# Kernel tuning notes

Measured on AMD Instinct MI355X. Metric: run time of the kernel, lower is better.

The kernel has to match this reference:

```python
import jax, jax.numpy as jnp
import numpy as np

VOCAB = 10000
EMB = 512
D_IMG = 2048
RNN = 1024
SEQ_LEN = 16
START_TOKEN = VOCAB + 1  # 10001
V_OUT = VOCAB + 3        # 10003


def setup_inputs() -> dict:
    key = jax.random.key(0)
    ks = jax.random.split(key, 24)
    g = lambda k, shape, fan_in: jax.random.normal(k, shape, jnp.float32) / np.sqrt(fan_in)
    inp = {
        "img_features": jax.random.normal(ks[0], (64, 196, D_IMG), jnp.float32),
        "captions": jax.random.randint(ks[1], (64, SEQ_LEN), 0, VOCAB),
        # embedding table
        "emb": g(ks[2], (V_OUT, EMB), EMB),
        # LSTMCell (PyTorch gate order i,f,g,o), stored as [in, 4H]
        "Wih": g(ks[3], (EMB + D_IMG, 4 * RNN), EMB + D_IMG),
        "Whh": g(ks[4], (RNN, 4 * RNN), RNN),
        "bih": jnp.zeros((4 * RNN,), jnp.float32),
        "bhh": jnp.zeros((4 * RNN,), jnp.float32),
        # init_h / init_c
        "Wh0": g(ks[5], (D_IMG, RNN), D_IMG), "bh0": jnp.zeros((RNN,), jnp.float32),
        "Wc0": g(ks[6], (D_IMG, RNN), D_IMG), "bc0": jnp.zeros((RNN,), jnp.float32),
        # f_beta gate
        "Wfb": g(ks[7], (RNN, D_IMG), RNN), "bfb": jnp.zeros((D_IMG,), jnp.float32),
        # deep_output
        "Wout": g(ks[8], (RNN, V_OUT), RNN), "bout": jnp.zeros((V_OUT,), jnp.float32),
        # attention: U (rnn->rnn), W (img->rnn), v (rnn->1)
        "WU": g(ks[9], (RNN, RNN), RNN), "bU": jnp.zeros((RNN,), jnp.float32),
        "WW": g(ks[10], (D_IMG, RNN), D_IMG), "bW": jnp.zeros((RNN,), jnp.float32),
        "Wv": g(ks[11], (RNN, 1), RNN), "bv": jnp.zeros((1,), jnp.float32),
    }
    return inp


def reference(img_features, captions, emb, Wih, Whh, bih, bhh, Wh0, bh0, Wc0, bc0,
              Wfb, bfb, Wout, bout, WU, bU, WW, bW, Wv, bv):
    B = img_features.shape[0]
    # get_target: prepend START token -> [B, T+1]
    start = jnp.full((B, 1), START_TOKEN, dtype=captions.dtype)
    target = jnp.concatenate([start, captions], axis=1)
    embedding = emb[target]                      # [B, T+1, EMB]
    emb_seq = jnp.transpose(embedding, (1, 0, 2))  # [T+1, B, EMB]

    # init LSTM state from mean image features
    avg = img_features.mean(axis=1)              # [B, D_IMG]
    h0 = jnp.tanh(avg @ Wh0 + bh0)
    c0 = jnp.tanh(avg @ Wc0 + bc0)

    # image-side attention projection is timestep-independent
    W_s = img_features @ WW + bW                 # [B, L, RNN]
    b_gates = bih + bhh

    def step(carry, emb_t):
        h, c = carry
        # additive attention
        U_h = h @ WU + bU                        # [B, RNN]
        att = jnp.tanh(W_s + U_h[:, None, :])    # [B, L, RNN]
        e = (att @ Wv).squeeze(-1) + bv          # [B, L]
        alpha = jax.nn.softmax(e, axis=1)
        context = jnp.einsum('bld,bl->bd', img_features, alpha)  # [B, D_IMG]
        gate = jax.nn.sigmoid(h @ Wfb + bfb)
        x = jnp.concatenate([emb_t, gate * context], axis=1)     # [B, EMB+D_IMG]
        # LSTMCell, PyTorch gate order i,f,g,o
        gates = x @ Wih + h @ Whh + b_gates      # [B, 4*RNN]
        i, f, gg, o = jnp.split(gates, 4, axis=1)
        c_new = jax.nn.sigmoid(f) * c + jax.nn.sigmoid(i) * jnp.tanh(gg)
        h_new = jax.nn.sigmoid(o) * jnp.tanh(c_new)
        out = h_new @ Wout + bout                # [B, V_OUT] (dropout=identity, eval mode)
        return (h_new, c_new), (out, alpha)

    (_, _), (preds_t, alphas_t) = jax.lax.scan(step, (h0, c0), emb_seq)
    preds = jnp.transpose(preds_t, (1, 0, 2))    # [B, T+1, V_OUT]
    alphas = jnp.transpose(alphas_t, (1, 0, 2))  # [B, T+1, L]
    return preds, alphas
```

## Files before the change

### kernel.cpp

```cpp
#include <hip/hip_runtime.h>
#include <cstdint>

#define NB    64
#define LIMG  196
#define DIMG  2048
#define RNND  1024
#define EMBD  512
#define TSTEPS 17
#define VOUTD 10003

typedef short bf16x8 __attribute__((ext_vector_type(8)));
typedef float f32x4  __attribute__((ext_vector_type(4)));

__device__ __forceinline__ float fast_sig(float x) {
    return 1.f / (1.f + __expf(-x));
}
__device__ __forceinline__ float fast_tanh(float x) {
    float ax = fabsf(x);
    float e  = __expf(2.f * ax);
    float r  = 1.f - 2.f / (e + 1.f);
    return copysignf(r, x);
}
__device__ __forceinline__ void split_bf(float x, short& hi, short& lo) {
    unsigned u  = __float_as_uint(x);
    unsigned hb = u & 0xffff0000u;
    hi = (short)(u >> 16);
    float r = x - __uint_as_float(hb);
    lo = (short)(__float_as_uint(r) >> 16);
}

__global__ __launch_bounds__(256) void tsplit(
    const float* __restrict__ S1, int ld1,
    const float* __restrict__ S2, int ld2,
    short* __restrict__ outh, short* __restrict__ outl,
    int N, int K, int ksplit, int nsplit)
{
    __shared__ float T[64][65];
    const int k0 = blockIdx.x * 64, n0 = blockIdx.y * 64;
    const int tid = threadIdx.x;
    const int rr = tid >> 2;
    const int cc = (tid & 3) * 16;
    const int kk = k0 + rr;
    const int nn = n0 + cc;
    const float* rp; int col;
    if (nsplit > 0) {
        if (nn >= nsplit) { rp = S2 + (size_t)kk * ld2; col = nn - nsplit; }
        else              { rp = S1 + (size_t)kk * ld1; col = nn; }
    } else {
        if (kk < ksplit)  { rp = S1 + (size_t)kk * ld1; col = nn; }
        else              { rp = S2 + (size_t)(kk - ksplit) * ld2; col = nn; }
    }
#pragma unroll
    for (int j = 0; j < 16; j++)
        T[rr][cc + j] = (nn + j < N) ? rp[col + j] : 0.f;
    __syncthreads();
    const int wn = tid >> 2;
    const int wk = (tid & 3) * 16;
    const int gn = n0 + wn;
    if (gn >= N) return;
    bf16x8 h0, h1, l0, l1;
#pragma unroll
    for (int j = 0; j < 8; j++) {
        short hh, ll;
        split_bf(T[wk + j][wn], hh, ll);     h0[j] = hh; l0[j] = ll;
        split_bf(T[wk + 8 + j][wn], hh, ll); h1[j] = hh; l1[j] = ll;
    }
    const size_t o = (size_t)gn * K + k0 + wk;
    *(bf16x8*)&outh[o]     = h0;
    *(bf16x8*)&outh[o + 8] = h1;
    *(bf16x8*)&outl[o]     = l0;
    *(bf16x8*)&outl[o + 8] = l1;
}

__global__ __launch_bounds__(256) void gemm_mt(
    const float* __restrict__ Af,
    const short* __restrict__ Ah16, const short* __restrict__ Al16,
    const short* __restrict__ Bh16, const short* __restrict__ Bl16,
    const float* __restrict__ bias, float* __restrict__ C,
    int N, int K, int lda, int ldb, int ldc, int pmap)
{
    __shared__ short Ah[64 * 40], Al[64 * 40];
    __shared__ short Bh[128 * 40], Bl[128 * 40];

    const int tid = threadIdx.x;
    const int n0  = blockIdx.x * 128;
    const int m0  = blockIdx.y * 64;

    const int lane = tid & 63;
    const int w    = tid >> 6;
    const int wn   = w * 32;
    const int lm   = lane & 15;
    const int lk   = lane >> 4;

    const int a_r = tid >> 2;
    const int a_c = (tid & 3) * 8;
    const int b_r = tid >> 1;
    const int b_c = (tid & 1) * 16;

    f32x4 acc[4][2];
#pragma unroll
    for (int i = 0; i < 4; i++)
#pragma unroll
        for (int j = 0; j < 2; j++) acc[i][j] = (f32x4)0.f;

    bf16x8 rah, ral, rbh0, rbh1, rbl0, rbl1;
    auto load_tile = [&](int k0) {
        if (Af) {
            const float* ap = Af + (size_t)(m0 + a_r) * lda + (k0 + a_c);
            float4 q0 = *(const float4*)(ap);
            float4 q1 = *(const float4*)(ap + 4);
            float f[8] = {q0.x, q0.y, q0.z, q0.w, q1.x, q1.y, q1.z, q1.w};
#pragma unroll
            for (int j = 0; j < 8; j++) {
                short hh, ll;
                split_bf(f[j], hh, ll); rah[j] = hh; ral[j] = ll;
            }
        } else {
            rah = *(const bf16x8*)(Ah16 + (size_t)(m0 + a_r) * lda + (k0 + a_c));
            ral = *(const bf16x8*)(Al16 + (size_t)(m0 + a_r) * lda + (k0 + a_c));
        }
        const short* pb = Bh16 + (size_t)(n0 + b_r) * ldb + (k0 + b_c);
        rbh0 = *(const bf16x8*)pb; rbh1 = *(const bf16x8*)(pb + 8);
        const short* qb = Bl16 + (size_t)(n0 + b_r) * ldb + (k0 + b_c);
        rbl0 = *(const bf16x8*)qb; rbl1 = *(const bf16x8*)(qb + 8);
    };

    load_tile(0);
    for (int k0 = 0; k0 < K; k0 += 32) {
        __syncthreads();
        *(bf16x8*)&Ah[a_r * 40 + a_c] = rah;
        *(bf16x8*)&Al[a_r * 40 + a_c] = ral;
        *(bf16x8*)&Bh[b_r * 40 + b_c]     = rbh0;
        *(bf16x8*)&Bh[b_r * 40 + b_c + 8] = rbh1;
        *(bf16x8*)&Bl[b_r * 40 + b_c]     = rbl0;
        *(bf16x8*)&Bl[b_r * 40 + b_c + 8] = rbl1;
        __syncthreads();
        if (k0 + 32 < K) load_tile(k0 + 32);

        bf16x8 afh[4], afl[4], bfh[2], bfl[2];
#pragma unroll
        for (int fm = 0; fm < 4; fm++) {
            const int idx = (fm * 16 + lm) * 40 + lk * 8;
            afh[fm] = *(bf16x8*)&Ah[idx];
            afl[fm] = *(bf16x8*)&Al[idx];
        }
#pragma unroll
        for (int fn = 0; fn < 2; fn++) {
            const int idx = (wn + fn * 16 + lm) * 40 + lk * 8;
            bfh[fn] = *(bf16x8*)&Bh[idx];
            bfl[fn] = *(bf16x8*)&Bl[idx];
        }
#pragma unroll
        for (int fm = 0; fm < 4; fm++)
#pragma unroll
            for (int fn = 0; fn < 2; fn++) {
                acc[fm][fn] = __builtin_amdgcn_mfma_f32_16x16x32_bf16(afh[fm], bfh[fn], acc[fm][fn], 0, 0, 0);
                acc[fm][fn] = __builtin_amdgcn_mfma_f32_16x16x32_bf16(afh[fm], bfl[fn], acc[fm][fn], 0, 0, 0);
                acc[fm][fn] = __builtin_amdgcn_mfma_f32_16x16x32_bf16(afl[fm], bfh[fn], acc[fm][fn], 0, 0, 0);
            }
    }

#pragma unroll
    for (int fm = 0; fm < 4; fm++)
#pragma unroll
        for (int fn = 0; fn < 2; fn++) {
            const int col = n0 + wn + fn * 16 + lm;
            if (col >= N) continue;
            const float bb = bias ? bias[col] : 0.f;
#pragma unroll
            for (int r = 0; r < 4; r++) {
                const int row = m0 + fm * 16 + lk * 4 + r;
                const size_t orow = pmap ? (size_t)((row & 63) * TSTEPS + (row >> 6))
                                         : (size_t)row;
                C[orow * ldc + col] = acc[fm][fn][r] + bb;
            }
        }
}

__global__ __launch_bounds__(256) void gemm_sk(
    const float* __restrict__ A,
    const short* __restrict__ Bh16, const short* __restrict__ Bl16,
    float* __restrict__ P, int N, int K, int lda, int ldb, int Kc)
{
    __shared__ short Ah[64 * 40], Al[64 * 40];
    __shared__ short Bh[128 * 40], Bl[128 * 40];

    const int tid = threadIdx.x;
    const int n0  = blockIdx.x * 128;
    const int s   = blockIdx.z;
    const int kb  = s * Kc;

    const int lane = tid & 63;
    const int w    = tid >> 6;
    const int wn   = w * 32;
    const int lm   = lane & 15;
    const int lk   = lane >> 4;

    const int a_r = tid >> 2;
    const int a_c = (tid & 3) * 8;
    const int b_r = tid >> 1;
    const int b_c = (tid & 1) * 16;

    f32x4 acc[4][2];
#pragma unroll
    for (int i = 0; i < 4; i++)
#pragma unroll
        for (int j = 0; j < 2; j++) acc[i][j] = (f32x4)0.f;

    for (int k0 = kb; k0 < kb + Kc; k0 += 32) {
        const float* ap = A + (size_t)a_r * lda + (k0 + a_c);
        float4 q0 = *(const float4*)(ap);
        float4 q1 = *(const float4*)(ap + 4);
        float f[8] = {q0.x, q0.y, q0.z, q0.w, q1.x, q1.y, q1.z, q1.w};
        bf16x8 ah, al;
#pragma unroll
        for (int j = 0; j < 8; j++) {
            short hh, ll;
            split_bf(f[j], hh, ll); ah[j] = hh; al[j] = ll;
        }
        const short* pb = Bh16 + (size_t)(n0 + b_r) * ldb + (k0 + b_c);
        bf16x8 bh0 = *(const bf16x8*)pb, bh1 = *(const bf16x8*)(pb + 8);
        const short* qb = Bl16 + (size_t)(n0 + b_r) * ldb + (k0 + b_c);
        bf16x8 bl0 = *(const bf16x8*)qb, bl1 = *(const bf16x8*)(qb + 8);

        __syncthreads();
        *(bf16x8*)&Ah[a_r * 40 + a_c] = ah;
        *(bf16x8*)&Al[a_r * 40 + a_c] = al;
        *(bf16x8*)&Bh[b_r * 40 + b_c]     = bh0;
        *(bf16x8*)&Bh[b_r * 40 + b_c + 8] = bh1;
        *(bf16x8*)&Bl[b_r * 40 + b_c]     = bl0;
        *(bf16x8*)&Bl[b_r * 40 + b_c + 8] = bl1;
        __syncthreads();

        bf16x8 afh[4], afl[4], bfh[2], bfl[2];
#pragma unroll
        for (int fm = 0; fm < 4; fm++) {
            const int idx = (fm * 16 + lm) * 40 + lk * 8;
            afh[fm] = *(bf16x8*)&Ah[idx];
            afl[fm] = *(bf16x8*)&Al[idx];
        }
#pragma unroll
        for (int fn = 0; fn < 2; fn++) {
            const int idx = (wn + fn * 16 + lm) * 40 + lk * 8;
            bfh[fn] = *(bf16x8*)&Bh[idx];
            bfl[fn] = *(bf16x8*)&Bl[idx];
        }
#pragma unroll
        for (int fm = 0; fm < 4; fm++)
#pragma unroll
            for (int fn = 0; fn < 2; fn++) {
                acc[fm][fn] = __builtin_amdgcn_mfma_f32_16x16x32_bf16(afh[fm], bfh[fn], acc[fm][fn], 0, 0, 0);
                acc[fm][fn] = __builtin_amdgcn_mfma_f32_16x16x32_bf16(afh[fm], bfl[fn], acc[fm][fn], 0, 0, 0);
                acc[fm][fn] = __builtin_amdgcn_mfma_f32_16x16x32_bf16(afl[fm], bfh[fn], acc[fm][fn], 0, 0, 0);
            }
    }

    float* Ps = P + (size_t)s * 64 * N;
#pragma unroll
    for (int fm = 0; fm < 4; fm++)
#pragma unroll
        for (int fn = 0; fn < 2; fn++) {
            const int col = n0 + wn + fn * 16 + lm;
#pragma unroll
            for (int r = 0; r < 4; r++) {
                const int row = fm * 16 + lk * 4 + r;
                Ps[(size_t)row * N + col] = acc[fm][fn][r];
            }
        }
}

__global__ __launch_bounds__(256) void gemm64(
    const float* __restrict__ A, const float* __restrict__ B,
    const float* __restrict__ bias, float* __restrict__ C,
    int N, int K, int Kc, int ldc, int act, int direct)
{
    __shared__ float As[16][64];
    __shared__ float Bs[16][68];

    const int tid = threadIdx.x;
    const int n0  = blockIdx.x * 64;
    const int m0  = blockIdx.y * 64;
    const int s   = blockIdx.z;
    const int kb  = s * Kc;
    const int ke  = min(K, kb + Kc);

    const int tm = (tid >> 4) << 2;
    const int tn = (tid & 15) << 2;

    float acc[4][4];
#pragma unroll
    for (int i = 0; i < 4; i++)
#pragma unroll
        for (int j = 0; j < 4; j++) acc[i][j] = 0.f;

    const int a_m = tid >> 2;
    const int a_k = (tid & 3) << 2;
    const int b_k = tid >> 4;
    const int b_n = (tid & 15) << 2;
    const bool n4 = ((N & 3) == 0);

    for (int k0 = kb; k0 < ke; k0 += 16) {
        float4 av = *(const float4*)(A + (size_t)(m0 + a_m) * K + (k0 + a_k));
        float4 bv;
        {
            const int nn = n0 + b_n;
            const float* brow = B + (size_t)(k0 + b_k) * N;
            if (n4) {
                bv = (nn < N) ? *(const float4*)(brow + nn) : make_float4(0.f,0.f,0.f,0.f);
            } else {
                bv.x = (nn + 0 < N) ? brow[nn + 0] : 0.f;
                bv.y = (nn + 1 < N) ? brow[nn + 1] : 0.f;
                bv.z = (nn + 2 < N) ? brow[nn + 2] : 0.f;
                bv.w = (nn + 3 < N) ? brow[nn + 3] : 0.f;
            }
        }
        __syncthreads();
        As[a_k + 0][a_m] = av.x;
        As[a_k + 1][a_m] = av.y;
        As[a_k + 2][a_m] = av.z;
        As[a_k + 3][a_m] = av.w;
        *(float4*)&Bs[b_k][b_n] = bv;
        __syncthreads();
#pragma unroll
        for (int k = 0; k < 16; k++) {
            float4 a4 = *(const float4*)&As[k][tm];
            float4 b4 = *(const float4*)&Bs[k][tn];
            acc[0][0] = fmaf(a4.x, b4.x, acc[0][0]);
            acc[0][1] = fmaf(a4.x, b4.y, acc[0][1]);
            acc[0][2] = fmaf(a4.x, b4.z, acc[0][2]);
            acc[0][3] = fmaf(a4.x, b4.w, acc[0][3]);
            acc[1][0] = fmaf(a4.y, b4.x, acc[1][0]);
            acc[1][1] = fmaf(a4.y, b4.y, acc[1][1]);
            acc[1][2] = fmaf(a4.y, b4.z, acc[1][2]);
            acc[1][3] = fmaf(a4.y, b4.w, acc[1][3]);
            acc[2][0] = fmaf(a4.z, b4.x, acc[2][0]);
            acc[2][1] = fmaf(a4.z, b4.y, acc[2][1]);
            acc[2][2] = fmaf(a4.z, b4.z, acc[2][2]);
            acc[2][3] = fmaf(a4.z, b4.w, acc[2][3]);
            acc[3][0] = fmaf(a4.w, b4.x, acc[3][0]);
            acc[3][1] = fmaf(a4.w, b4.y, acc[3][1]);
            acc[3][2] = fmaf(a4.w, b4.z, acc[3][2]);
            acc[3][3] = fmaf(a4.w, b4.w, acc[3][3]);
        }
    }

    if (direct) {
#pragma unroll
        for (int i = 0; i < 4; i++) {
            const int m = m0 + tm + i;
            const size_t row = (size_t)m * ldc;
#pragma unroll
            for (int j = 0; j < 4; j++) {
                const int n = n0 + tn + j;
                if (n < N) {
                    float v = acc[i][j] + (bias ? bias[n] : 0.f);
                    if (act == 1) v = fast_tanh(v);
                    else if (act == 2) v = fast_sig(v);
                    C[row + n] = v;
                }
            }
        }
    } else {
        float* Pp = C + (size_t)s * 64 * N;
#pragma unroll
        for (int i = 0; i < 4; i++) {
#pragma unroll
            for (int j = 0; j < 4; j++) {
                const int n = n0 + tn + j;
                if (n < N) Pp[(size_t)(tm + i) * N + n] = acc[i][j];
            }
        }
    }
}

__global__ __launch_bounds__(256) void gemm_mfma3(
    const float* __restrict__ A, const float* __restrict__ B,
    const float* __restrict__ bias, float* __restrict__ C,
    int M, int N, int K, int lda, int ldb, int ldc, int pmap)
{
    __shared__ short Ah[128 * 40], Al[128 * 40];
    __shared__ short Bh[128 * 40], Bl[128 * 40];

    const int tid = threadIdx.x;
    const int n0  = blockIdx.x * 128;
    const int m0  = blockIdx.y * 128;

    const int lane = tid & 63;
    const int w    = tid >> 6;
    const int wm   = (w >> 1) * 64;
    const int wn   = (w & 1) * 64;
    const int lm   = lane & 15;
    const int lk   = lane >> 4;

    const int ar = tid >> 1;
    const int ac = (tid & 1) * 16;
    const int kb = (tid & 15) * 2;
    const int c8 = (tid >> 4) * 8;

    const bool bvec = ((ldb & 3) == 0) && (n0 + 128 <= N);

    f32x4 acc[4][4];
#pragma unroll
    for (int i = 0; i < 4; i++)
#pragma unroll
        for (int j = 0; j < 4; j++) acc[i][j] = (f32x4)0.f;

    for (int k0 = 0; k0 < K; k0 += 32) {
        float f[16];
        if (m0 + ar < M) {
            const float* ap = A + (size_t)(m0 + ar) * lda + (k0 + ac);
            float4 q0 = *(const float4*)(ap);
            float4 q1 = *(const float4*)(ap + 4);
            float4 q2 = *(const float4*)(ap + 8);
            float4 q3 = *(const float4*)(ap + 12);
            f[0]=q0.x; f[1]=q0.y; f[2]=q0.z; f[3]=q0.w;
            f[4]=q1.x; f[5]=q1.y; f[6]=q1.z; f[7]=q1.w;
            f[8]=q2.x; f[9]=q2.y; f[10]=q2.z; f[11]=q2.w;
            f[12]=q3.x; f[13]=q3.y; f[14]=q3.z; f[15]=q3.w;
        } else {
#pragma unroll
            for (int j = 0; j < 16; j++) f[j] = 0.f;
        }
        bf16x8 h0, h1, l0, l1;
#pragma unroll
        for (int j = 0; j < 8; j++) {
            short hh, ll;
            split_bf(f[j], hh, ll);     h0[j] = hh; l0[j] = ll;
            split_bf(f[8 + j], hh, ll); h1[j] = hh; l1[j] = ll;
        }
        float g0[8], g1[8];
        if (bvec) {
            const float* bp0 = B + (size_t)(k0 + kb) * ldb + (n0 + c8);
            const float* bp1 = bp0 + ldb;
            float4 q0 = *(const float4*)(bp0);
            float4 q1 = *(const float4*)(bp0 + 4);
            float4 q2 = *(const float4*)(bp1);
            float4 q3 = *(const float4*)(bp1 + 4);
            g0[0]=q0.x; g0[1]=q0.y; g0[2]=q0.z; g0[3]=q0.w;
            g0[4]=q1.x; g0[5]=q1.y; g0[6]=q1.z; g0[7]=q1.w;
            g1[0]=q2.x; g1[1]=q2.y; g1[2]=q2.z; g1[3]=q2.w;
            g1[4]=q3.x; g1[5]=q3.y; g1[6]=q3.z; g1[7]=q3.w;
        } else {
            const float* bp0 = B + (size_t)(k0 + kb) * ldb;
            const float* bp1 = bp0 + ldb;
#pragma unroll
            for (int j = 0; j < 8; j++) {
                const int nn = n0 + c8 + j;
                g0[j] = (nn < N) ? bp0[nn] : 0.f;
                g1[j] = (nn < N) ? bp1[nn] : 0.f;
            }
        }
        __syncthreads();
        *(bf16x8*)&Ah[ar * 40 + ac]     = h0;
        *(bf16x8*)&Ah[ar * 40 + ac + 8] = h1;
        *(bf16x8*)&Al[ar * 40 + ac]     = l0;
        *(bf16x8*)&Al[ar * 40 + ac + 8] = l1;
#pragma unroll
        for (int j = 0; j < 8; j++) {
            short ha, la, hb, lb;
            split_bf(g0[j], ha, la);
            split_bf(g1[j], hb, lb);
            const int ci = (c8 + j) * 40 + kb;
            *(int*)&Bh[ci] = (int)((unsigned short)ha | ((unsigned)(unsigned short)hb << 16));
            *(int*)&Bl[ci] = (int)((unsigned short)la | ((unsigned)(unsigned short)lb << 16));
        }
        __syncthreads();

        bf16x8 afh[4], afl[4], bfh[4], bfl[4];
#pragma unroll
        for (int fm = 0; fm < 4; fm++) {
            const int idx = (wm + fm * 16 + lm) * 40 + lk * 8;
            afh[fm] = *(bf16x8*)&Ah[idx];
            afl[fm] = *(bf16x8*)&Al[idx];
        }
#pragma unroll
        for (int fn = 0; fn < 4; fn++) {
            const int idx = (wn + fn * 16 + lm) * 40 + lk * 8;
            bfh[fn] = *(bf16x8*)&Bh[idx];
            bfl[fn] = *(bf16x8*)&Bl[idx];
        }
#pragma unroll
        for (int fm = 0; fm < 4; fm++)
#pragma unroll
            for (int fn = 0; fn < 4; fn++) {
                acc[fm][fn] = __builtin_amdgcn_mfma_f32_16x16x32_bf16(afh[fm], bfh[fn], acc[fm][fn], 0, 0, 0);
                acc[fm][fn] = __builtin_amdgcn_mfma_f32_16x16x32_bf16(afh[fm], bfl[fn], acc[fm][fn], 0, 0, 0);
                acc[fm][fn] = __builtin_amdgcn_mfma_f32_16x16x32_bf16(afl[fm], bfh[fn], acc[fm][fn], 0, 0, 0);
            }
    }

#pragma unroll
    for (int fm = 0; fm < 4; fm++) {
#pragma unroll
        for (int fn = 0; fn < 4; fn++) {
            const int col = n0 + wn + fn * 16 + lm;
            if (col >= N) continue;
            const float bb = bias ? bias[col] : 0.f;
#pragma unroll
            for (int r = 0; r < 4; r++) {
                const int row = m0 + wm + fm * 16 + lk * 4 + r;
                if (row >= M) continue;
                const size_t orow = pmap ? (size_t)((row & 63) * TSTEPS + (row >> 6))
                                         : (size_t)row;
                C[orow * ldc + col] = acc[fm][fn][r] + bb;
            }
        }
    }
}

__global__ __launch_bounds__(256) void reduce_partials(
    const float* __restrict__ P, int S, int N,
    const float* __restrict__ bias, float* __restrict__ C, int ldc, int act)
{
    const int idx = blockIdx.x * 256 + threadIdx.x;
    const int total = 64 * N;
    if (idx >= total) return;
    const int m = idx / N;
    const int n = idx - m * N;
    float v = bias ? bias[n] : 0.f;
    for (int s = 0; s < S; s++) v += P[(size_t)s * total + idx];
    if (act == 1) v = fast_tanh(v);
    else if (act == 2) v = fast_sig(v);
    else if (act == 3 && n >= RNND) v = fast_sig(v);
    C[(size_t)m * ldc + n] = v;
}

__global__ __launch_bounds__(256) void reduce_lstm(
    const float* __restrict__ P, int S, const float* __restrict__ bsum,
    float* __restrict__ hn, float* __restrict__ c,
    short* __restrict__ hbh, short* __restrict__ hbl)
{
    const int idx = blockIdx.x * 256 + threadIdx.x;
    const int b = idx >> 10, r = idx & 1023;
    const float* pb = P + (size_t)b * 4096;
    float gi = bsum[r], gf = bsum[1024 + r], gg = bsum[2048 + r], go = bsum[3072 + r];
    for (int s = 0; s < S; s++) {
        const float* q = pb + (size_t)s * 64 * 4096;
        gi += q[r]; gf += q[1024 + r]; gg += q[2048 + r]; go += q[3072 + r];
    }
    const float ig = fast_sig(gi);
    const float fg = fast_sig(gf);
    const float g2 = fast_tanh(gg);
    const float og = fast_sig(go);
    const float cn = fg * c[idx] + ig * g2;
    const float hv = og * fast_tanh(cn);
    c[idx]  = cn;
    hn[idx] = hv;
    if (hbh) {
        short hi, lo;
        split_bf(hv, hi, lo);
        hbh[idx] = hi;
        hbl[idx] = lo;
    }
}

__global__ __launch_bounds__(256) void mean_img(
    const float* __restrict__ img, float* __restrict__ avg)
{
    const int b = blockIdx.x;
    const int d = blockIdx.y * 256 + threadIdx.x;
    const float* p = img + (size_t)b * LIMG * DIMG + d;
    float s = 0.f;
    for (int l = 0; l < LIMG; l++) s += p[(size_t)l * DIMG];
    avg[(size_t)b * DIMG + d] = s * (1.f / 196.f);
}

__global__ __launch_bounds__(256) void concat_w(
    const float* __restrict__ WU, const float* __restrict__ Wfb,
    float* __restrict__ Wug)
{
    const int idx = blockIdx.x * 256 + threadIdx.x;
    if (idx >= 1024 * 3072) return;
    const int k = idx / 3072;
    const int j = idx - k * 3072;
    Wug[idx] = (j < 1024) ? WU[(size_t)k * 1024 + j] : Wfb[(size_t)k * 2048 + (j - 1024)];
}

__global__ __launch_bounds__(256) void concat_b(
    const float* __restrict__ bU, const float* __restrict__ bfb,
    const float* __restrict__ bih, const float* __restrict__ bhh,
    float* __restrict__ bug, float* __restrict__ bsum)
{
    const int j = blockIdx.x * 256 + threadIdx.x;
    if (j < 3072) bug[j] = (j < 1024) ? bU[j] : bfb[j - 1024];
    if (j < 4096) bsum[j] = bih[j] + bhh[j];
}

__global__ __launch_bounds__(256) void attn_e(
    const float* __restrict__ Ws, const float* __restrict__ ug,
    const float* __restrict__ Wv, const float* __restrict__ bv,
    float* __restrict__ e)
{
    const int wv   = (blockIdx.x << 2) + (threadIdx.x >> 6);
    const int lane = threadIdx.x & 63;
    const int b    = wv / LIMG;
    const float* wrow = Ws + (size_t)wv * RNND;
    const float* urow = ug + (size_t)b * 3072;
    float acc = 0.f;
#pragma unroll
    for (int k = lane * 4; k < RNND; k += 256) {
        float4 wq = *(const float4*)(wrow + k);
        float4 uq = *(const float4*)(urow + k);
        float4 vq = *(const float4*)(Wv + k);
        acc += fast_tanh(wq.x + uq.x) * vq.x + fast_tanh(wq.y + uq.y) * vq.y
             + fast_tanh(wq.z + uq.z) * vq.z + fast_tanh(wq.w + uq.w) * vq.w;
    }
#pragma unroll
    for (int off = 32; off > 0; off >>= 1) acc += __shfl_down(acc, off);
    if (lane == 0) e[wv] = acc + bv[0];
}

__global__ __launch_bounds__(256) void ctx_fuse(
    const float* __restrict__ e, const float* __restrict__ img,
    const float* __restrict__ ug, const float* __restrict__ embt,
    const int* __restrict__ captions, const float* __restrict__ h,
    float* __restrict__ x, float* __restrict__ alphas_out, int t)
{
    __shared__ float al[256];
    __shared__ float red[256];
    const int b = blockIdx.x, y = blockIdx.y, tid = threadIdx.x;

    const float v = (tid < LIMG) ? e[b * LIMG + tid] : -3.0e38f;
    red[tid] = v; __syncthreads();
    for (int s = 128; s > 0; s >>= 1) {
        if (tid < s) red[tid] = fmaxf(red[tid], red[tid + s]);
        __syncthreads();
    }
    const float mx = red[0]; __syncthreads();
    const float ex = (tid < LIMG) ? __expf(v - mx) : 0.f;
    red[tid] = ex; __syncthreads();
    for (int s = 128; s > 0; s >>= 1) {
        if (tid < s) red[tid] += red[tid + s];
        __syncthreads();
    }
    const float inv = 1.f / red[0];
    al[tid] = ex * inv;
    __syncthreads();

    if (y == 0) {
        if (tid < LIMG)
            alphas_out[(size_t)b * (TSTEPS * LIMG) + t * LIMG + tid] = al[tid];
        const int tok = (t == 0) ? 10001 : captions[b * 16 + (t - 1)];
        for (int j = tid; j < EMBD; j += 256)
            x[(size_t)b * 3584 + j] = embt[(size_t)tok * EMBD + j];
        for (int j = tid; j < RNND; j += 256)
            x[(size_t)b * 3584 + 2560 + j] = h[(size_t)b * RNND + j];
    } else {
        const int d0 = (y - 1) * 512 + tid * 2;
        const float* ib = img + (size_t)b * LIMG * DIMG + d0;
        float a0 = 0.f, a1 = 0.f;
#pragma unroll 4
        for (int l = 0; l < LIMG; l++) {
            float2 q = *(const float2*)(ib + (size_t)l * DIMG);
            a0 = fmaf(al[l], q.x, a0);
            a1 = fmaf(al[l], q.y, a1);
        }
        const float g0 = ug[(size_t)b * 3072 + 1024 + d0];
        const float g1 = ug[(size_t)b * 3072 + 1024 + d0 + 1];
        x[(size_t)b * 3584 + EMBD + d0]     = g0 * a0;
        x[(size_t)b * 3584 + EMBD + d0 + 1] = g1 * a1;
    }
}

__global__ __launch_bounds__(256) void softmax_alpha(
    const float* __restrict__ e, float* __restrict__ alpha,
    float* __restrict__ alphas_out, int t)
{
    __shared__ float red[256];
    const int b = blockIdx.x, tid = threadIdx.x;
    const float v = (tid < LIMG) ? e[b * LIMG + tid] : -3.0e38f;
    red[tid] = v; __syncthreads();
    for (int s = 128; s > 0; s >>= 1) {
        if (tid < s) red[tid] = fmaxf(red[tid], red[tid + s]);
        __syncthreads();
    }
    const float mx = red[0]; __syncthreads();
    const float ex = (tid < LIMG) ? __expf(v - mx) : 0.f;
    red[tid] = ex; __syncthreads();
    for (int s = 128; s > 0; s >>= 1) {
        if (tid < s) red[tid] += red[tid + s];
        __syncthreads();
    }
    const float inv = 1.f / red[0];
    if (tid < LIMG) {
        const float a = ex * inv;
        alpha[b * LIMG + tid] = a;
        alphas_out[(size_t)b * (TSTEPS * LIMG) + t * LIMG + tid] = a;
    }
}

__global__ __launch_bounds__(128) void assemble_x(
    const float* __restrict__ img, const float* __restrict__ alpha,
    const float* __restrict__ ug, const float* __restrict__ emb,
    const int* __restrict__ captions, const float* __restrict__ h,
    float* __restrict__ x, int t, int stride)
{
    const int b = blockIdx.x, y = blockIdx.y, tid = threadIdx.x;
    if (y < 4) {
        const int tok = (t == 0) ? 10001 : captions[b * 16 + (t - 1)];
        const int j = y * 128 + tid;
        x[(size_t)b * stride + j] = emb[(size_t)tok * EMBD + j];
    } else if (y < 20) {
        __shared__ float al[LIMG];
        for (int i = tid; i < LIMG; i += 128) al[i] = alpha[b * LIMG + i];
        __syncthreads();
        const int d = (y - 4) * 128 + tid;
        const float* ib = img + (size_t)b * LIMG * DIMG + d;
        float accv = 0.f;
#pragma unroll 4
        for (int l = 0; l < LIMG; l++) accv = fmaf(al[l], ib[(size_t)l * DIMG], accv);
        const float g = ug[(size_t)b * 3072 + 1024 + d];
        x[(size_t)b * stride + EMBD + d] = g * accv;
    } else {
        const int j = (y - 20) * 128 + tid;
        x[(size_t)b * stride + 2560 + j] = h[(size_t)b * RNND + j];
    }
}

extern "C" void kernel_launch(void* const* d_in, const int* in_sizes, int n_in,
                              void* d_out, int out_size, void* d_ws, size_t ws_size,
                              hipStream_t stream)
{
    const float* img      = (const float*)d_in[0];
    const int*   captions = (const int*)d_in[1];
    const float* emb      = (const float*)d_in[2];
    const float* Wih      = (const float*)d_in[3];
    const float* Whh      = (const float*)d_in[4];
    const float* bih      = (const float*)d_in[5];
    const float* bhh      = (const float*)d_in[6];
    const float* Wh0      = (const float*)d_in[7];
    const float* bh0      = (const float*)d_in[8];
    const float* Wc0      = (const float*)d_in[9];
    const float* bc0      = (const float*)d_in[10];
    const float* Wfb      = (const float*)d_in[11];
    const float* bfb      = (const float*)d_in[12];
    const float* Wout     = (const float*)d_in[13];
    const float* bout     = (const float*)d_in[14];
    const float* WU       = (const float*)d_in[15];
    const float* bU       = (const float*)d_in[16];
    const float* WW       = (const float*)d_in[17];
    const float* bW       = (const float*)d_in[18];
    const float* Wv       = (const float*)d_in[19];
    const float* bv       = (const float*)d_in[20];

    float* preds      = (float*)d_out;
    float* alphas_out = preds + (size_t)NB * TSTEPS * VOUTD;

    const size_t NEED = 190000000;

    if (ws_size >= NEED) {
        float* w = (float*)d_ws;
        float* Ws    = w; w += (size_t)12544 * 1024;
        float* ug    = w; w += (size_t)64 * 3072;
        float* P     = w; w += (size_t)8 * 64 * 4096;
        float* e     = w; w += (size_t)64 * LIMG;
        float* alpha = w; w += (size_t)64 * LIMG;
        float* xh    = w; w += (size_t)64 * 3584;
        float* h     = w; w += (size_t)64 * RNND;
        float* c     = w; w += (size_t)64 * RNND;
        float* avg   = w; w += (size_t)64 * DIMG;
        float* bsum  = w; w += 4096;
        float* bug   = w; w += 3072;
        short* u = (short*)w;
        short* Hbh     = u; u += (size_t)1280 * 1024;
        short* Hbl     = u; u += (size_t)1280 * 1024;
        short* WWTh    = u; u += (size_t)1024 * 2048;
        short* WWTl    = u; u += (size_t)1024 * 2048;
        short* WugTh   = u; u += (size_t)3072 * 1024;
        short* WugTl   = u; u += (size_t)3072 * 1024;
        short* WfullTh = u; u += (size_t)4096 * 3584;
        short* WfullTl = u; u += (size_t)4096 * 3584;
        short* WoutTh  = u; u += (size_t)10112 * 1024;
        short* WoutTl  = u; u += (size_t)10112 * 1024;

        mean_img<<<dim3(NB, 8), 256, 0, stream>>>(img, avg);
        gemm64<<<dim3(16, 1, 8), 256, 0, stream>>>(avg, Wh0, nullptr, P, 1024, 2048, 256, 0, 0, 0);
        reduce_partials<<<256, 256, 0, stream>>>(P, 8, 1024, bh0, h, 1024, 1);
        gemm64<<<dim3(16, 1, 8), 256, 0, stream>>>(avg, Wc0, nullptr, P, 1024, 2048, 256, 0, 0, 0);
        reduce_partials<<<256, 256, 0, stream>>>(P, 8, 1024, bc0, c, 1024, 1);
        concat_b<<<16, 256, 0, stream>>>(bU, bfb, bih, bhh, bug, bsum);

        tsplit<<<dim3(32, 16), 256, 0, stream>>>(WW, 1024, WW, 1024, WWTh, WWTl, 1024, 2048, 2048, 0);
        tsplit<<<dim3(16, 48), 256, 0, stream>>>(WU, 1024, Wfb, 2048, WugTh, WugTl, 3072, 1024, 1024, 1024);
        tsplit<<<dim3(56, 64), 256, 0, stream>>>(Wih, 4096, Whh, 4096, WfullTh, WfullTl, 4096, 3584, 2560, 0);
        tsplit<<<dim3(16, 157), 256, 0, stream>>>(Wout, VOUTD, Wout, VOUTD, WoutTh, WoutTl, VOUTD, 1024, 1024, 0);

        gemm_mt<<<dim3(8, 196), 256, 0, stream>>>(img, nullptr, nullptr, WWTh, WWTl,
                                                  bW, Ws, 1024, 2048, 2048, 2048, 1024, 0);

        for (int t = 0; t < TSTEPS; t++) {
            gemm_sk<<<dim3(24, 1, 8), 256, 0, stream>>>(h, WugTh, WugTl, P, 3072, 1024, 1024, 1024, 128);
            reduce_partials<<<768, 256, 0, stream>>>(P, 8, 3072, bug, ug, 3072, 3);
            attn_e<<<3136, 256, 0, stream>>>(Ws, ug, Wv, bv, e);
            ctx_fuse<<<dim3(NB, 5), 256, 0, stream>>>(e, img, ug, emb, captions, h, xh, alphas_out, t);
            gemm_sk<<<dim3(32, 1, 7), 256, 0, stream>>>(xh, WfullTh, WfullTl, P, 4096, 3584, 3584, 3584, 512);
            reduce_lstm<<<256, 256, 0, stream>>>(P, 7, bsum, h, c,
                                                 Hbh + (size_t)(t + 1) * 65536,
                                                 Hbl + (size_t)(t + 1) * 65536);
        }

        gemm_mt<<<dim3(79, 17), 256, 0, stream>>>(nullptr, Hbh + 65536, Hbl + 65536,
                                                  WoutTh, WoutTl, bout, preds,
                                                  VOUTD, 1024, 1024, 1024, VOUTD, 1);
    } else {
        float* w = (float*)d_ws;
        float* Ws    = w; w += (size_t)12544 * 1024;
        float* ug    = w; w += (size_t)64 * 3072;
        float* P     = w; w += (size_t)12 * 64 * 4096;
        float* e     = w; w += (size_t)64 * LIMG;
        float* alpha = w; w += (size_t)64 * LIMG;
        float* x     = w; w += (size_t)64 * 2560;
        float* Hh    = w; w += (size_t)18 * 64 * RNND;
        float* c     = w; w += (size_t)64 * RNND;
        float* avg   = w; w += (size_t)64 * DIMG;
        float* bsum  = w; w += 4096;
        float* Wug   = w; w += (size_t)1024 * 3072;
        float* bug   = w; w += 3072;

        mean_img<<<dim3(NB, 8), 256, 0, stream>>>(img, avg);
        gemm64<<<dim3(16, 1, 8), 256, 0, stream>>>(avg, Wh0, nullptr, P, 1024, 2048, 256, 0, 0, 0);
        reduce_partials<<<256, 256, 0, stream>>>(P, 8, 1024, bh0, Hh, 1024, 1);
        gemm64<<<dim3(16, 1, 8), 256, 0, stream>>>(avg, Wc0, nullptr, P, 1024, 2048, 256, 0, 0, 0);
        reduce_partials<<<256, 256, 0, stream>>>(P, 8, 1024, bc0, c, 1024, 1);
        concat_b<<<16, 256, 0, stream>>>(bU, bfb, bih, bhh, bug, bsum);
        concat_w<<<12288, 256, 0, stream>>>(WU, Wfb, Wug);
        gemm_mfma3<<<dim3(8, 98), 256, 0, stream>>>(img, WW, bW, Ws,
                                                    12544, 1024, 2048, 2048, 1024, 1024, 0);
        for (int t = 0; t < TSTEPS; t++) {
            const float* hc = Hh + (size_t)t * 64 * RNND;
            float*       hn = Hh + (size_t)(t + 1) * 64 * RNND;
            gemm64<<<dim3(48, 1, 8), 256, 0, stream>>>(hc, Wug, nullptr, P, 3072, 1024, 128, 0, 0, 0);
            reduce_partials<<<768, 256, 0, stream>>>(P, 8, 3072, bug, ug, 3072, 3);
            attn_e<<<3136, 256, 0, stream>>>(Ws, ug, Wv, bv, e);
            softmax_alpha<<<NB, 256, 0, stream>>>(e, alpha, alphas_out, t);
            assemble_x<<<dim3(NB, 20), 128, 0, stream>>>(img, alpha, ug, emb, captions, hc, x, t, 2560);
            gemm64<<<dim3(64, 1, 8), 256, 0, stream>>>(x, Wih, nullptr, P, 4096, 2560, 320, 0, 0, 0);
            gemm64<<<dim3(64, 1, 4), 256, 0, stream>>>(hc, Whh, nullptr, P + (size_t)8 * 64 * 4096,
                                                       4096, 1024, 256, 0, 0, 0);
            reduce_lstm<<<256, 256, 0, stream>>>(P, 12, bsum, hn, c, nullptr, nullptr);
        }
        gemm_mfma3<<<dim3(79, 9), 256, 0, stream>>>(Hh + (size_t)64 * RNND, Wout, bout, preds,
                                                    TSTEPS * 64, VOUTD, 1024, 1024, VOUTD, VOUTD, 1);
    }
}
```

Before: 1.891 ms.

## Fuse partial reduction, attention scores, softmax and context into one kernel

Replaces the per-step reduce_partials, attn_e and ctx_fuse launches with a single attn_mega kernel that uses one 1024-thread block per batch row. Each block sums the split-K partials, computes attention energies over the 196 image locations, applies the softmax, and builds the gated context plus the embedding and h slices of the LSTM input. This removes two launches per timestep and the global round-trips of ug and e. In exchange, the bandwidth-heavy reads of Ws and img now run on only 64 blocks instead of thousands, which cuts parallelism and may leave most CUs idle.

```diff
diff --git a/kernel.cpp b/kernel.cpp
--- a/kernel.cpp
+++ b/kernel.cpp
@@ -267,6 +267,115 @@
                 Ps[(size_t)row * N + col] = acc[fm][fn][r];
             }
         }
+}
+
+__global__ __launch_bounds__(1024) void attn_mega(
+    const float* __restrict__ P, const float* __restrict__ bug,
+    const float* __restrict__ Ws, const float* __restrict__ Wv,
+    const float* __restrict__ bv, const float* __restrict__ img,
+    const float* __restrict__ embt, const int* __restrict__ captions,
+    const float* __restrict__ h, float* __restrict__ xh,
+    float* __restrict__ alphas_out, int t)
+{
+    __shared__ float uh[1024];
+    __shared__ float gg[2048];
+    __shared__ float ee[256];
+    __shared__ float red[256];
+
+    const int b = blockIdx.x, tid = threadIdx.x;
+
+    {
+        const float* pb = P + (size_t)b * 3072;
+        float v = bug[tid];
+        float g0 = bug[1024 + tid];
+        float g1 = bug[2048 + tid];
+#pragma unroll
+        for (int s = 0; s < 8; s++) {
+            const float* q = pb + (size_t)s * 64 * 3072;
+            v  += q[tid];
+            g0 += q[1024 + tid];
+            g1 += q[2048 + tid];
+        }
+        uh[tid] = v;
+        gg[tid] = fast_sig(g0);
+        gg[tid + 1024] = fast_sig(g1);
+
+        const int tok = (t == 0) ? 10001 : captions[b * 16 + (t - 1)];
+        if (tid < EMBD) xh[(size_t)b * 3584 + tid] = embt[(size_t)tok * EMBD + tid];
+        xh[(size_t)b * 3584 + 2560 + tid] = h[(size_t)b * RNND + tid];
+    }
+    __syncthreads();
+
+    {
+        const int wave = tid >> 6, lane = tid & 63;
+        float ur[16], vr[16];
+#pragma unroll
+        for (int j = 0; j < 4; j++) {
+            const int k = lane * 4 + j * 256;
+            float4 u4 = *(const float4*)&uh[k];
+            float4 v4 = *(const float4*)(Wv + k);
+            ur[j*4+0] = u4.x; ur[j*4+1] = u4.y; ur[j*4+2] = u4.z; ur[j*4+3] = u4.w;
+            vr[j*4+0] = v4.x; vr[j*4+1] = v4.y; vr[j*4+2] = v4.z; vr[j*4+3] = v4.w;
+        }
+        for (int l = wave; l < LIMG; l += 16) {
+            const float* wrow = Ws + ((size_t)b * LIMG + l) * RNND;
+            float acc = 0.f;
+#pragma unroll
+            for (int j = 0; j < 4; j++) {
+                const int k = lane * 4 + j * 256;
+                float4 wq = *(const float4*)(wrow + k);
+                acc += fast_tanh(wq.x + ur[j*4+0]) * vr[j*4+0]
+                     + fast_tanh(wq.y + ur[j*4+1]) * vr[j*4+1]
+                     + fast_tanh(wq.z + ur[j*4+2]) * vr[j*4+2]
+                     + fast_tanh(wq.w + ur[j*4+3]) * vr[j*4+3];
+            }
+#pragma unroll
+            for (int off = 32; off > 0; off >>= 1) acc += __shfl_down(acc, off);
+            if (lane == 0) ee[l] = acc + bv[0];
+        }
+    }
+    __syncthreads();
+
+    {
+        if (tid < 256) red[tid] = (tid < LIMG) ? ee[tid] : -3.0e38f;
+        __syncthreads();
+        for (int s = 128; s > 0; s >>= 1) {
+            if (tid < s) red[tid] = fmaxf(red[tid], red[tid + s]);
+            __syncthreads();
+        }
+        const float mx = red[0];
+        __syncthreads();
+        float ex = 0.f;
+        if (tid < LIMG) ex = __expf(ee[tid] - mx);
+        if (tid < 256) red[tid] = ex;
+        __syncthreads();
+        for (int s = 128; s > 0; s >>= 1) {
+            if (tid < s) red[tid] += red[tid + s];
+            __syncthreads();
+        }
+        const float inv = 1.f / red[0];
+        __syncthreads();
+        if (tid < LIMG) {
+            const float a = ex * inv;
+            ee[tid] = a;
+            alphas_out[(size_t)b * (TSTEPS * LIMG) + t * LIMG + tid] = a;
+        }
+    }
+    __syncthreads();
+
+    {
+        const int d0 = tid * 2;
+        const float* ib = img + (size_t)b * LIMG * DIMG + d0;
+        float a0 = 0.f, a1 = 0.f;
+#pragma unroll 4
+        for (int l = 0; l < LIMG; l++) {
+            float2 q = *(const float2*)(ib + (size_t)l * DIMG);
+            a0 = fmaf(ee[l], q.x, a0);
+            a1 = fmaf(ee[l], q.y, a1);
+        }
+        xh[(size_t)b * 3584 + EMBD + d0]     = gg[d0] * a0;
+        xh[(size_t)b * 3584 + EMBD + d0 + 1] = gg[d0 + 1] * a1;
+    }
 }
 
 __global__ __launch_bounds__(256) void gemm64(
@@ -608,58 +717,6 @@
 #pragma unroll
     for (int off = 32; off > 0; off >>= 1) acc += __shfl_down(acc, off);
     if (lane == 0) e[wv] = acc + bv[0];
-}
-
-__global__ __launch_bounds__(256) void ctx_fuse(
-    const float* __restrict__ e, const float* __restrict__ img,
-    const float* __restrict__ ug, const float* __restrict__ embt,
-    const int* __restrict__ captions, const float* __restrict__ h,
-    float* __restrict__ x, float* __restrict__ alphas_out, int t)
-{
-    __shared__ float al[256];
-    __shared__ float red[256];
-    const int b = blockIdx.x, y = blockIdx.y, tid = threadIdx.x;
-
-    const float v = (tid < LIMG) ? e[b * LIMG + tid] : -3.0e38f;
-    red[tid] = v; __syncthreads();
-    for (int s = 128; s > 0; s >>= 1) {
-        if (tid < s) red[tid] = fmaxf(red[tid], red[tid + s]);
-        __syncthreads();
-    }
-    const float mx = red[0]; __syncthreads();
-    const float ex = (tid < LIMG) ? __expf(v - mx) : 0.f;
-    red[tid] = ex; __syncthreads();
-    for (int s = 128; s > 0; s >>= 1) {
-        if (tid < s) red[tid] += red[tid + s];
-        __syncthreads();
-    }
-    const float inv = 1.f / red[0];
-    al[tid] = ex * inv;
-    __syncthreads();
-
-    if (y == 0) {
-        if (tid < LIMG)
-            alphas_out[(size_t)b * (TSTEPS * LIMG) + t * LIMG + tid] = al[tid];
-        const int tok = (t == 0) ? 10001 : captions[b * 16 + (t - 1)];
-        for (int j = tid; j < EMBD; j += 256)
-            x[(size_t)b * 3584 + j] = embt[(size_t)tok * EMBD + j];
-        for (int j = tid; j < RNND; j += 256)
-            x[(size_t)b * 3584 + 2560 + j] = h[(size_t)b * RNND + j];
-    } else {
-        const int d0 = (y - 1) * 512 + tid * 2;
-        const float* ib = img + (size_t)b * LIMG * DIMG + d0;
-        float a0 = 0.f, a1 = 0.f;
-#pragma unroll 4
-        for (int l = 0; l < LIMG; l++) {
-            float2 q = *(const float2*)(ib + (size_t)l * DIMG);
-            a0 = fmaf(al[l], q.x, a0);
-            a1 = fmaf(al[l], q.y, a1);
-        }
-        const float g0 = ug[(size_t)b * 3072 + 1024 + d0];
-        const float g1 = ug[(size_t)b * 3072 + 1024 + d0 + 1];
-        x[(size_t)b * 3584 + EMBD + d0]     = g0 * a0;
-        x[(size_t)b * 3584 + EMBD + d0 + 1] = g1 * a1;
-    }
 }
 
 __global__ __launch_bounds__(256) void softmax_alpha(
@@ -790,9 +847,8 @@
 
         for (int t = 0; t < TSTEPS; t++) {
             gemm_sk<<<dim3(24, 1, 8), 256, 0, stream>>>(h, WugTh, WugTl, P, 3072, 1024, 1024, 1024, 128);
-            reduce_partials<<<768, 256, 0, stream>>>(P, 8, 3072, bug, ug, 3072, 3);
-            attn_e<<<3136, 256, 0, stream>>>(Ws, ug, Wv, bv, e);
-            ctx_fuse<<<dim3(NB, 5), 256, 0, stream>>>(e, img, ug, emb, captions, h, xh, alphas_out, t);
+            attn_mega<<<NB, 1024, 0, stream>>>(P, bug, Ws, Wv, bv, img, emb, captions,
+                                               h, xh, alphas_out, t);
             gemm_sk<<<dim3(32, 1, 7), 256, 0, stream>>>(xh, WfullTh, WfullTl, P, 4096, 3584, 3584, 3584, 512);
             reduce_lstm<<<256, 256, 0, stream>>>(P, 7, bsum, h, c,
                                                  Hbh + (size_t)(t + 1) * 65536,
```

Measured after the change: 2.262 ms. 1.2x slower.
